# Kernel tuning notes

Hardware: AMD Instinct MI355X
Metric: run time of the kernel (lower is better)

Reference implementation:

```python
import jax, jax.numpy as jnp
import numpy as np

L, E, H, C, N = 3, 512, 8, 64, 65536
DH = E // H
LN_EPS = 1e-5


def setup_inputs() -> dict:
    key = jax.random.key(0)
    ks = jax.random.split(key, 10)
    s = 1.0 / np.sqrt(E)
    return {
        "support_features": jax.random.normal(ks[0], (N, E), jnp.float32),
        "support_labels": jax.random.randint(ks[1], (N,), 0, C),
        "W1": jax.random.normal(ks[2], (L, E, E), jnp.float32) * s,
        "b1": jnp.zeros((L, E), jnp.float32),
        "gamma": jnp.ones((L, E), jnp.float32),
        "beta": jnp.zeros((L, E), jnp.float32),
        "W2": jax.random.normal(ks[3], (L, E, E), jnp.float32) * s,
        "b2": jnp.zeros((L, E), jnp.float32),
        "Wq": jax.random.normal(ks[4], (E, E), jnp.float32) * s,
        "bq": jnp.zeros((E,), jnp.float32),
        "Wk": jax.random.normal(ks[5], (E, E), jnp.float32) * s,
        "bk": jnp.zeros((E,), jnp.float32),
        "Wv": jax.random.normal(ks[6], (E, E), jnp.float32) * s,
        "bv": jnp.zeros((E,), jnp.float32),
        "Wo": jax.random.normal(ks[7], (E, E), jnp.float32) * s,
        "bo": jnp.zeros((E,), jnp.float32),
        "level_weights": jnp.ones((L,), jnp.float32) / L,
        "level_temps": jnp.ones((L,), jnp.float32),
    }


def _layer_norm(x, g, b):
    mu = jnp.mean(x, axis=-1, keepdims=True)
    var = jnp.var(x, axis=-1, keepdims=True)
    return (x - mu) * jax.lax.rsqrt(var + LN_EPS) * g + b


def reference(support_features, support_labels, W1, b1, gamma, beta, W2, b2,
              Wq, bq, Wk, bk, Wv, bv, Wo, bo, level_weights, level_temps):
    # class membership mask [C, N]; segment counts [C]
    onehot = support_labels[None, :] == jnp.arange(C)[:, None]
    counts = jnp.sum(onehot, axis=1).astype(support_features.dtype)
    scale = 1.0 / np.sqrt(DH)
    protos = []
    for l in range(L):  # small fixed number of levels
        # prototype MLP (dropout inactive at eval)
        h = jnp.maximum(_layer_norm(support_features @ W1[l] + b1[l], gamma[l], beta[l]), 0.0)
        feat = h @ W2[l] + b2[l]                              # [N, E]
        # per-class mean context (segment mean) -> query
        ctx = (onehot.astype(feat.dtype) @ feat) / counts[:, None]  # [C, E]
        q = (ctx @ Wq + bq).reshape(C, H, DH)
        k = (feat @ Wk + bk).reshape(N, H, DH)
        v = (feat @ Wv + bv).reshape(N, H, DH)
        scores = jnp.einsum('chd,nhd->chn', q, k) * scale      # [C, H, N]
        scores = jnp.where(onehot[:, None, :], scores, -jnp.inf)
        attn = jax.nn.softmax(scores, axis=-1)
        out = jnp.einsum('chn,nhd->chd', attn, v).reshape(C, E)
        protos.append(out @ Wo + bo)                           # [C, E]
    lw = jax.nn.softmax(level_weights)
    final = protos[0] * (lw[0] / level_temps[0])
    for i in range(1, L):
        final = final + protos[i] * (lw[i] / level_temps[i])
    return final
```

## Files before the change

kernel.cpp:

```cpp
#include <hip/hip_runtime.h>
#include <math.h>

#define N_SUP 65536
#define E_DIM 512
#define H_HEADS 8
#define C_CLS 64
#define DHD 64
#define L_LEV 3
#define LN_EPS 1e-5f
#define ATTN_SPLITS 8
#define CTX_SPLITS 16
#define SCAT_BLOCKS 256
#define KV_LD 1024

typedef _Float16 f16x8 __attribute__((ext_vector_type(8)));
typedef _Float16 f16x4 __attribute__((ext_vector_type(4)));
typedef float f32x4 __attribute__((ext_vector_type(4)));

__device__ __forceinline__ void gload_lds16(const void* g, void* lds) {
    __builtin_amdgcn_global_load_lds((const __attribute__((address_space(1))) void*)g,
                                     (__attribute__((address_space(3))) void*)lds,
                                     16, 0, 0);
}

__global__ __launch_bounds__(512, 2)
void hgemm256(const _Float16* __restrict__ A, int lda, size_t aStride,
              const _Float16* __restrict__ Bt, size_t btStride,
              const float* __restrict__ bias, size_t biasStride,
              _Float16* __restrict__ C, int ldc, size_t cStride, int nCol) {
    const int z = blockIdx.y;
    A += z * aStride; Bt += z * btStride; bias += z * biasStride; C += z * cStride;

    const int nRow = gridDim.x / nCol;
    const int R = nRow < 64 ? nRow : 64;
    const int bid = blockIdx.x;
    const int bandSz = R * nCol;
    const int band = bid / bandSz;
    const int rem = bid % bandSz;
    const int colT = rem / R;
    const int rowT = band * R + (rem % R);
    const int row0 = rowT * 256, col0 = colT * 256;

    __shared__ _Float16 smem[2][2][256][64];

    const int tid = threadIdx.x;
    const int wave = tid >> 6, lane = tid & 63;
    const int wm2 = (wave & 1) * 128;
    const int wn4 = (wave >> 1) * 64;
    const int m = lane & 15, q = lane >> 4;

    const int sr = tid >> 3;
    const int sb = tid & 7;
    const int sblk = sb ^ (sr & 7);

    const _Float16* Asrc = A + (size_t)(row0 + sr) * lda + sblk * 8;
    const _Float16* Bsrc = Bt + (size_t)(col0 + sr) * E_DIM + sblk * 8;
    const size_t aPass = (size_t)64 * lda;
    const size_t bPass = (size_t)64 * E_DIM;

#define STAGE_TILE(k0, s)                                                     \
    {                                                                         \
        char* la = (char*)&smem[s][0][0][0] + wave * 1024;                    \
        char* lb = (char*)&smem[s][1][0][0] + wave * 1024;                    \
        _Pragma("unroll")                                                     \
        for (int p = 0; p < 4; ++p)                                           \
            gload_lds16(Asrc + (size_t)p * aPass + (k0), la + p * 8192);      \
        _Pragma("unroll")                                                     \
        for (int p = 0; p < 4; ++p)                                           \
            gload_lds16(Bsrc + (size_t)p * bPass + (k0), lb + p * 8192);      \
    }

    f32x4 acc[8][4];
#pragma unroll
    for (int i = 0; i < 8; ++i)
#pragma unroll
        for (int j = 0; j < 4; ++j) acc[i][j] = (f32x4){0.f, 0.f, 0.f, 0.f};

    const int c0k = ((q) ^ (m & 7)) * 8;
    const int c1k = ((4 + q) ^ (m & 7)) * 8;

    STAGE_TILE(0, 0);
    STAGE_TILE(64, 1);

    for (int t = 0; t < 8; ++t) {
        const int s = t & 1;
        if (t < 7) {
            asm volatile("s_waitcnt vmcnt(8)" ::: "memory");
        } else {
            asm volatile("s_waitcnt vmcnt(0)" ::: "memory");
        }
        __builtin_amdgcn_s_barrier();

        const _Float16* As = &smem[s][0][0][0];
        const _Float16* Bs = &smem[s][1][0][0];

        f16x8 a0[8], a1[8], b0[4], b1[4];
#pragma unroll
        for (int fr = 0; fr < 8; ++fr) {
            const int rb = (wm2 + fr * 16 + m) * 64;
            a0[fr] = *(const f16x8*)&As[rb + c0k];
            a1[fr] = *(const f16x8*)&As[rb + c1k];
        }
#pragma unroll
        for (int fc = 0; fc < 4; ++fc) {
            const int rb = (wn4 + fc * 16 + m) * 64;
            b0[fc] = *(const f16x8*)&Bs[rb + c0k];
            b1[fc] = *(const f16x8*)&Bs[rb + c1k];
        }
        asm volatile("s_waitcnt lgkmcnt(0)" ::: "memory");
        __builtin_amdgcn_s_barrier();

        if (t + 2 < 8) {
            const int k0n = (t + 2) * 64;
            STAGE_TILE(k0n, s);
        }

        __builtin_amdgcn_s_setprio(1);
#pragma unroll
        for (int fr = 0; fr < 8; ++fr)
#pragma unroll
            for (int fc = 0; fc < 4; ++fc)
                acc[fr][fc] = __builtin_amdgcn_mfma_f32_16x16x32_f16(a0[fr], b0[fc], acc[fr][fc], 0, 0, 0);
#pragma unroll
        for (int fr = 0; fr < 8; ++fr)
#pragma unroll
            for (int fc = 0; fc < 4; ++fc)
                acc[fr][fc] = __builtin_amdgcn_mfma_f32_16x16x32_f16(a1[fr], b1[fc], acc[fr][fc], 0, 0, 0);
        __builtin_amdgcn_s_setprio(0);
    }
#undef STAGE_TILE

#pragma unroll
    for (int fr = 0; fr < 8; ++fr) {
        const int rbase = row0 + wm2 + fr * 16 + q * 4;
#pragma unroll
        for (int fc = 0; fc < 4; ++fc) {
            const int col = col0 + wn4 + fc * 16 + m;
            const float bv = bias[col];
#pragma unroll
            for (int r = 0; r < 4; ++r)
                C[(size_t)(rbase + r) * ldc + col] = (_Float16)(acc[fr][fc][r] + bv);
        }
    }
}

__global__ __launch_bounds__(256)
void conv32to16(const float* __restrict__ in, _Float16* __restrict__ out, int n4) {
    int i = blockIdx.x * 256 + threadIdx.x;
    if (i < n4) {
        f32x4 v = ((const f32x4*)in)[i];
        f16x4 o = {(_Float16)v[0], (_Float16)v[1], (_Float16)v[2], (_Float16)v[3]};
        ((f16x4*)out)[i] = o;
    }
}

__global__ __launch_bounds__(256)
void transpose_all(const float* __restrict__ W1, const float* __restrict__ Wk,
                   const float* __restrict__ Wv, const float* __restrict__ Wq,
                   _Float16* __restrict__ W1allT, _Float16* __restrict__ WkvqT) {
    const int z = blockIdx.z;
    const float* src;
    _Float16* dst;
    const size_t MSZ = (size_t)E_DIM * E_DIM;
    if (z < 3)       { src = W1 + z * MSZ; dst = W1allT + z * MSZ; }
    else if (z == 3) { src = Wk;           dst = WkvqT; }
    else if (z == 4) { src = Wv;           dst = WkvqT + MSZ; }
    else             { src = Wq;           dst = WkvqT + 2 * MSZ; }

    __shared__ float t[32][33];
    const int k0 = blockIdx.x * 32, n0 = blockIdx.y * 32;
    const int tx = threadIdx.x & 31, ty = threadIdx.x >> 5;
#pragma unroll
    for (int r = 0; r < 32; r += 8)
        t[ty + r][tx] = src[(size_t)(k0 + ty + r) * E_DIM + n0 + tx];
    __syncthreads();
#pragma unroll
    for (int r = 0; r < 32; r += 8)
        dst[(size_t)(n0 + ty + r) * E_DIM + k0 + tx] = (_Float16)t[tx][ty + r];
}

__global__ __launch_bounds__(256)
void bias_compose(const float* __restrict__ b2, const float* __restrict__ Wk,
                  const float* __restrict__ Wv, const float* __restrict__ Wq,
                  const float* __restrict__ bk, const float* __restrict__ bv,
                  const float* __restrict__ bq, float* __restrict__ bcomp) {
    const int l = blockIdx.y;
    const int n = blockIdx.x * 256 + threadIdx.x;
    const float* W; const float* bb; int nn;
    if (n < 512)       { W = Wk; bb = bk; nn = n; }
    else if (n < 1024) { W = Wv; bb = bv; nn = n - 512; }
    else               { W = Wq; bb = bq; nn = n - 1024; }
    float acc = 0.f;
    for (int j = 0; j < E_DIM; ++j)
        acc = fmaf(b2[l * E_DIM + j], W[(size_t)j * E_DIM + nn], acc);
    bcomp[l * 1536 + n] = acc + bb[nn];
}

__global__ __launch_bounds__(256)
void ln_relu_all(_Float16* __restrict__ P, const float* __restrict__ gamma,
                 const float* __restrict__ beta) {
    const int row = blockIdx.x * 4 + (threadIdx.x >> 6);
    const int l = blockIdx.y;
    const int lane = threadIdx.x & 63;
    _Float16* prow = P + (size_t)row * (L_LEV * E_DIM) + l * E_DIM + lane * 8;
    const float* g = gamma + l * E_DIM + lane * 8;
    const float* b = beta  + l * E_DIM + lane * 8;
    f16x8 v = *(const f16x8*)prow;
    float x[8];
    float s = 0.f, s2 = 0.f;
#pragma unroll
    for (int e = 0; e < 8; ++e) {
        x[e] = (float)v[e];
        s += x[e];
        s2 = fmaf(x[e], x[e], s2);
    }
#pragma unroll
    for (int off = 32; off; off >>= 1) {
        s  += __shfl_xor(s, off);
        s2 += __shfl_xor(s2, off);
    }
    const float mean = s * (1.f / E_DIM);
    const float var  = s2 * (1.f / E_DIM) - mean * mean;
    const float rstd = rsqrtf(var + LN_EPS);
    f32x4 g0 = *(const f32x4*)g;
    f32x4 g1 = *(const f32x4*)(g + 4);
    f32x4 b0 = *(const f32x4*)b;
    f32x4 b1 = *(const f32x4*)(b + 4);
    f16x8 o;
#pragma unroll
    for (int e = 0; e < 4; ++e) {
        o[e]     = (_Float16)fmaxf(fmaf((x[e]     - mean) * rstd, g0[e], b0[e]), 0.f);
        o[e + 4] = (_Float16)fmaxf(fmaf((x[e + 4] - mean) * rstd, g1[e], b1[e]), 0.f);
    }
    *(f16x8*)prow = o;
}

__global__ __launch_bounds__(256)
void label_block_hist(const int* __restrict__ labels, int* __restrict__ blockCounts) {
    __shared__ int h[C_CLS];
    const int tid = threadIdx.x;
    if (tid < C_CLS) h[tid] = 0;
    __syncthreads();
    atomicAdd(&h[labels[blockIdx.x * 256 + tid]], 1);
    __syncthreads();
    if (tid < C_CLS) blockCounts[blockIdx.x * C_CLS + tid] = h[tid];
}

__global__ __launch_bounds__(64)
void scan_offsets(const int* __restrict__ blockCounts, int* __restrict__ counts,
                  int* __restrict__ offs, int* __restrict__ blockOffs) {
    const int c = threadIdx.x;
    int total = 0;
    for (int b = 0; b < SCAT_BLOCKS; ++b) total += blockCounts[b * C_CLS + c];
    counts[c] = total;
    __shared__ int tot[C_CLS];
    tot[c] = total;
    __syncthreads();
    int off = 0;
    for (int cc = 0; cc < c; ++cc) off += tot[cc];
    offs[c] = off;
    if (c == C_CLS - 1) offs[C_CLS] = off + total;
    int run = off;
    for (int b = 0; b < SCAT_BLOCKS; ++b) {
        blockOffs[b * C_CLS + c] = run;
        run += blockCounts[b * C_CLS + c];
    }
}

__global__ __launch_bounds__(256)
void scatter_sorted(const int* __restrict__ labels, const int* __restrict__ blockOffs,
                    int* __restrict__ members) {
    __shared__ int cur[C_CLS];
    const int tid = threadIdx.x;
    if (tid < C_CLS) cur[tid] = blockOffs[blockIdx.x * C_CLS + tid];
    __syncthreads();
    const int i = blockIdx.x * 256 + tid;
    const int c = labels[i];
    const int p = atomicAdd(&cur[c], 1);
    members[p] = i;
}

__global__ __launch_bounds__(256)
void zero_f32(float* __restrict__ p, int n) {
    int i = blockIdx.x * 256 + threadIdx.x;
    if (i < n) p[i] = 0.f;
}

__global__ __launch_bounds__(256)
void ctx_partial(const _Float16* __restrict__ P, const int* __restrict__ members,
                 const int* __restrict__ offsets, float* __restrict__ hpart) {
    const int c = blockIdx.x, split = blockIdx.y, l = blockIdx.z;
    const _Float16* src = P + (size_t)l * E_DIM;
    const int tid = threadIdx.x;
    const int wave = tid >> 6, lane = tid & 63;
    const int start = offsets[c], end = offsets[c + 1];
    const int wg = split * 4 + wave;
    const int stride = 4 * CTX_SPLITS;
    const int ld = L_LEV * E_DIM;

    float acc[8];
#pragma unroll
    for (int e = 0; e < 8; ++e) acc[e] = 0.f;

    int i = start + wg;
    for (; i + stride < end; i += 2 * stride) {
        const int n0 = members[i];
        const int n1 = members[i + stride];
        f16x8 r0 = *(const f16x8*)(src + (size_t)n0 * ld + lane * 8);
        f16x8 r1 = *(const f16x8*)(src + (size_t)n1 * ld + lane * 8);
#pragma unroll
        for (int e = 0; e < 8; ++e) acc[e] += (float)r0[e] + (float)r1[e];
    }
    if (i < end) {
        const int n0 = members[i];
        f16x8 r0 = *(const f16x8*)(src + (size_t)n0 * ld + lane * 8);
#pragma unroll
        for (int e = 0; e < 8; ++e) acc[e] += (float)r0[e];
    }

    __shared__ float red[4][64][8];
#pragma unroll
    for (int e = 0; e < 8; ++e) red[wave][lane][e] = acc[e];
    __syncthreads();
    float* dst = hpart + (((size_t)l * C_CLS + c) * CTX_SPLITS + split) * E_DIM;
#pragma unroll
    for (int t = 0; t < 2; ++t) {
        const int col = tid * 2 + t;
        const int ln = col >> 3, e = col & 7;
        dst[col] = red[0][ln][e] + red[1][ln][e] + red[2][ln][e] + red[3][ln][e];
    }
}

__global__ __launch_bounds__(256)
void row_gemm_q(const float* __restrict__ hpart, const int* __restrict__ counts,
                const _Float16* __restrict__ W2compT, const float* __restrict__ bcomp,
                float* __restrict__ q) {
    const int c = blockIdx.x, l = blockIdx.y;
    const int tid = threadIdx.x;
    const float inv = 1.f / (float)counts[c];
    __shared__ float xrow[E_DIM];
    const float* hp = hpart + ((size_t)l * C_CLS + c) * CTX_SPLITS * E_DIM;
    float s0 = 0.f, s1 = 0.f;
#pragma unroll
    for (int s = 0; s < CTX_SPLITS; ++s) {
        s0 += hp[s * E_DIM + tid];
        s1 += hp[s * E_DIM + tid + 256];
    }
    xrow[tid]       = s0 * inv;
    xrow[tid + 256] = s1 * inv;
    __syncthreads();

    const _Float16* Wq = W2compT + (size_t)l * 1536 * E_DIM + (size_t)1024 * E_DIM;
    const float* bias = bcomp + l * 1536 + 1024;
    const int n0 = tid, n1 = tid + 256;
    float a0 = 0.f, a1 = 0.f;
#pragma unroll 4
    for (int k0 = 0; k0 < E_DIM; k0 += 8) {
        f16x8 w0 = *(const f16x8*)(Wq + (size_t)n0 * E_DIM + k0);
        f16x8 w1 = *(const f16x8*)(Wq + (size_t)n1 * E_DIM + k0);
#pragma unroll
        for (int e = 0; e < 8; ++e) {
            const float xv = xrow[k0 + e];
            a0 = fmaf(xv, (float)w0[e], a0);
            a1 = fmaf(xv, (float)w1[e], a1);
        }
    }
    float* qq = q + (size_t)l * C_CLS * E_DIM;
    qq[c * E_DIM + n0] = a0 + bias[n0];
    qq[c * E_DIM + n1] = a1 + bias[n1];
}

__global__ __launch_bounds__(256)
void attn_partial(const float* __restrict__ q, const _Float16* __restrict__ kv,
                  const int* __restrict__ members, const int* __restrict__ offsets,
                  float* __restrict__ pm, float* __restrict__ pl,
                  float* __restrict__ po) {
    const int c = blockIdx.x, h = blockIdx.y, s = blockIdx.z;
    const int tid = threadIdx.x;
    const int wave = tid >> 6, lane = tid & 63;
    const int start = offsets[c], end = offsets[c + 1];
    const int g = s * 4 + wave;

    float qv[64];
    const bool active = (start + g * 64) < end;
    if (active) {
        const float* qrow = q + c * E_DIM + h * DHD;
#pragma unroll
        for (int d = 0; d < 64; ++d) qv[d] = qrow[d];
    }

    __shared__ float ps[4][64];
    float m = -INFINITY, lsum = 0.f, out = 0.f;

    for (int ch0 = start + g * 64; ch0 < end; ch0 += 4 * ATTN_SPLITS * 64) {
        const int nvalid = min(64, end - ch0);
        const int idx = ch0 + lane;
        const int mi = members[idx < end ? idx : end - 1];
        const _Float16* krow = kv + (size_t)mi * KV_LD + h * DHD;
        float dot = 0.f;
#pragma unroll
        for (int j = 0; j < 8; ++j) {
            f16x8 kr = *(const f16x8*)(krow + j * 8);
#pragma unroll
            for (int e = 0; e < 8; ++e)
                dot = fmaf((float)kr[e], qv[j * 8 + e], dot);
        }
        float sc = (lane < nvalid) ? dot * 0.125f : -INFINITY;
        float cm = sc;
#pragma unroll
        for (int off = 32; off; off >>= 1) cm = fmaxf(cm, __shfl_xor(cm, off));
        const float nm = fmaxf(m, cm);
        const float alpha = __expf(m - nm);
        const float p = (lane < nvalid) ? __expf(sc - nm) : 0.f;
        ps[wave][lane] = p;
        out *= alpha;
        lsum *= alpha;
        m = nm;
        asm volatile("" ::: "memory");
#pragma unroll 16
        for (int j = 0; j < 64; ++j) {
            const int nj = __shfl(mi, j);
            const float pj = ps[wave][j];
            const float vv = (float)kv[(size_t)nj * KV_LD + E_DIM + h * DHD + lane];
            out = fmaf(pj, vv, out);
            lsum += pj;
        }
    }

    __shared__ float rm[4], rl[4], racc[4][64];
    racc[wave][lane] = out;
    if (lane == 0) { rm[wave] = m; rl[wave] = lsum; }
    __syncthreads();
    if (wave == 0) {
        float M = fmaxf(fmaxf(rm[0], rm[1]), fmaxf(rm[2], rm[3]));
        float o = 0.f, Lt = 0.f;
#pragma unroll
        for (int w = 0; w < 4; ++w) {
            const float al = (rm[w] > -INFINITY) ? __expf(rm[w] - M) : 0.f;
            o  += al * racc[w][lane];
            Lt += al * rl[w];
        }
        const int pidx = (c * H_HEADS + h) * ATTN_SPLITS + s;
        po[pidx * 64 + lane] = o;
        if (lane == 0) { pm[pidx] = M; pl[pidx] = Lt; }
    }
}

__global__ __launch_bounds__(256)
void proto_accum(const float* __restrict__ pm, const float* __restrict__ pl,
                 const float* __restrict__ po, const float* __restrict__ Wo,
                 const float* __restrict__ bo, const float* __restrict__ lvlw,
                 const float* __restrict__ lvlt, int l, float* __restrict__ out) {
    const int c = blockIdx.x;
    const int tid = threadIdx.x;
    const int wave = tid >> 6, lane = tid & 63;
    __shared__ float xrow[E_DIM];
#pragma unroll
    for (int hh = wave; hh < H_HEADS; hh += 4) {
        const int ch = c * H_HEADS + hh;
        float M = -INFINITY;
#pragma unroll
        for (int s = 0; s < ATTN_SPLITS; ++s) M = fmaxf(M, pm[ch * ATTN_SPLITS + s]);
        float o = 0.f, Lt = 0.f;
#pragma unroll
        for (int s = 0; s < ATTN_SPLITS; ++s) {
            const int pidx = ch * ATTN_SPLITS + s;
            const float al = (pm[pidx] > -INFINITY) ? __expf(pm[pidx] - M) : 0.f;
            o  += al * po[pidx * 64 + lane];
            Lt += al * pl[pidx];
        }
        xrow[hh * 64 + lane] = o / Lt;
    }
    __syncthreads();

    float a0 = 0.f, a1 = 0.f;
#pragma unroll 8
    for (int k = 0; k < E_DIM; ++k) {
        float cv = xrow[k];
        a0 = fmaf(cv, Wo[(size_t)k * E_DIM + tid], a0);
        a1 = fmaf(cv, Wo[(size_t)k * E_DIM + tid + 256], a1);
    }
    float w0 = lvlw[0], w1 = lvlw[1], w2 = lvlw[2];
    float mx = fmaxf(w0, fmaxf(w1, w2));
    float e0 = expf(w0 - mx), e1 = expf(w1 - mx), e2 = expf(w2 - mx);
    float ssum = e0 + e1 + e2;
    float lw = (l == 0 ? e0 : (l == 1 ? e1 : e2)) / ssum;
    float coef = lw / lvlt[l];
    float r0 = (a0 + bo[tid]) * coef;
    float r1 = (a1 + bo[tid + 256]) * coef;
    if (l == 0) {
        out[c * E_DIM + tid]       = r0;
        out[c * E_DIM + tid + 256] = r1;
    } else {
        out[c * E_DIM + tid]       += r0;
        out[c * E_DIM + tid + 256] += r1;
    }
}

extern "C" void kernel_launch(void* const* d_in, const int* in_sizes, int n_in,
                              void* d_out, int out_size, void* d_ws, size_t ws_size,
                              hipStream_t stream) {
    const float* X      = (const float*)d_in[0];
    const int*   labels = (const int*)  d_in[1];
    const float* W1     = (const float*)d_in[2];
    const float* b1     = (const float*)d_in[3];
    const float* gamma  = (const float*)d_in[4];
    const float* beta   = (const float*)d_in[5];
    const float* W2     = (const float*)d_in[6];
    const float* b2     = (const float*)d_in[7];
    const float* Wq     = (const float*)d_in[8];
    const float* bq     = (const float*)d_in[9];
    const float* Wk     = (const float*)d_in[10];
    const float* bk     = (const float*)d_in[11];
    const float* Wv     = (const float*)d_in[12];
    const float* bv     = (const float*)d_in[13];
    const float* Wo     = (const float*)d_in[14];
    const float* bo     = (const float*)d_in[15];
    const float* lvlw   = (const float*)d_in[16];
    const float* lvlt   = (const float*)d_in[17];
    float* out = (float*)d_out;

    char* p = (char*)d_ws;
    const size_t MSZ = (size_t)E_DIM * E_DIM;
    _Float16* Xh      = (_Float16*)p; p += (size_t)N_SUP * E_DIM * 2;
    _Float16* bufPall = (_Float16*)p; p += (size_t)N_SUP * E_DIM * L_LEV * 2;
    _Float16* bufKV   = (_Float16*)p; p += (size_t)N_SUP * KV_LD * 2;
    _Float16* W1allT  = (_Float16*)p; p += L_LEV * MSZ * 2;
    _Float16* WkvqT   = (_Float16*)p; p += 3 * MSZ * 2;
    _Float16* W2f16   = (_Float16*)p; p += L_LEV * MSZ * 2;
    _Float16* W2compT = (_Float16*)p; p += (size_t)L_LEV * 1536 * E_DIM * 2;
    float* zeros512 = (float*)p; p += E_DIM * sizeof(float);
    float* bcomp = (float*)p; p += L_LEV * 1536 * sizeof(float);
    float* hpart = (float*)p; p += (size_t)L_LEV * C_CLS * CTX_SPLITS * E_DIM * sizeof(float);
    float* qb    = (float*)p; p += (size_t)L_LEV * C_CLS * E_DIM * sizeof(float);
    float* pm    = (float*)p; p += C_CLS * H_HEADS * ATTN_SPLITS * sizeof(float);
    float* pl    = (float*)p; p += C_CLS * H_HEADS * ATTN_SPLITS * sizeof(float);
    float* po    = (float*)p; p += (size_t)C_CLS * H_HEADS * ATTN_SPLITS * 64 * sizeof(float);
    int* counts      = (int*)p; p += 256;
    int* offs        = (int*)p; p += 512;
    int* members     = (int*)p; p += (size_t)N_SUP * sizeof(int);
    int* blockCounts = (int*)p; p += (size_t)SCAT_BLOCKS * C_CLS * sizeof(int);
    int* blockOffs   = (int*)p; p += (size_t)SCAT_BLOCKS * C_CLS * sizeof(int);

    label_block_hist<<<SCAT_BLOCKS, 256, 0, stream>>>(labels, blockCounts);
    scan_offsets<<<1, 64, 0, stream>>>(blockCounts, counts, offs, blockOffs);
    scatter_sorted<<<SCAT_BLOCKS, 256, 0, stream>>>(labels, blockOffs, members);

    conv32to16<<<(N_SUP * E_DIM / 4) / 256, 256, 0, stream>>>(X, Xh, N_SUP * E_DIM / 4);
    conv32to16<<<(int)(L_LEV * MSZ / 4 / 256), 256, 0, stream>>>(W2, W2f16, L_LEV * MSZ / 4);
    transpose_all<<<dim3(16, 16, 6), 256, 0, stream>>>(W1, Wk, Wv, Wq, W1allT, WkvqT);
    zero_f32<<<2, 256, 0, stream>>>(zeros512, E_DIM);

    hgemm256<<<dim3(6 * 2, L_LEV), 512, 0, stream>>>(
        WkvqT, E_DIM, 0, W2f16, MSZ, zeros512, 0,
        W2compT, E_DIM, (size_t)1536 * E_DIM, 2);
    bias_compose<<<dim3(6, L_LEV), 256, 0, stream>>>(b2, Wk, Wv, Wq, bk, bv, bq, bcomp);

    const int nRowT = N_SUP / 256;
    hgemm256<<<dim3(nRowT * 6, 1), 512, 0, stream>>>(
        Xh, E_DIM, 0, W1allT, 0, b1, 0, bufPall, L_LEV * E_DIM, 0, 6);
    ln_relu_all<<<dim3(N_SUP / 4, L_LEV), 256, 0, stream>>>(bufPall, gamma, beta);

    ctx_partial<<<dim3(C_CLS, CTX_SPLITS, L_LEV), 256, 0, stream>>>(
        bufPall, members, offs, hpart);
    row_gemm_q<<<dim3(C_CLS, L_LEV), 256, 0, stream>>>(
        hpart, counts, W2compT, bcomp, qb);

    for (int l = 0; l < L_LEV; ++l) {
        hgemm256<<<dim3(nRowT * 4, 1), 512, 0, stream>>>(
            bufPall + (size_t)l * E_DIM, L_LEV * E_DIM, 0,
            W2compT + (size_t)l * 1536 * E_DIM, 0,
            bcomp + l * 1536, 0, bufKV, KV_LD, 0, 4);
        attn_partial<<<dim3(C_CLS, H_HEADS, ATTN_SPLITS), 256, 0, stream>>>(
            qb + (size_t)l * C_CLS * E_DIM, bufKV, members, offs, pm, pl, po);
        proto_accum<<<C_CLS, 256, 0, stream>>>(pm, pl, po, Wo, bo, lvlw, lvlt, l, out);
    }
}
```

Before: 1.038 ms.

## Interleave LDS loads, global prefetch and MFMA in four sub-phases per k-tile

Restructures the fp16 MFMA GEMM main loop so each 64-wide k-tile is processed in four row-pair phases. Each phase loads a small slice of A fragments from LDS and issues part of the next tiles' global-to-LDS copies before running its MFMAs. This spreads memory traffic across the compute and reduces live A-fragment registers, at the cost of more barriers per tile and tighter vmcnt accounting.

```diff
diff --git a/kernel.cpp b/kernel.cpp
--- a/kernel.cpp
+++ b/kernel.cpp
@@ -58,17 +58,10 @@
     const size_t aPass = (size_t)64 * lda;
     const size_t bPass = (size_t)64 * E_DIM;
 
-#define STAGE_TILE(k0, s)                                                     \
-    {                                                                         \
-        char* la = (char*)&smem[s][0][0][0] + wave * 1024;                    \
-        char* lb = (char*)&smem[s][1][0][0] + wave * 1024;                    \
-        _Pragma("unroll")                                                     \
-        for (int p = 0; p < 4; ++p)                                           \
-            gload_lds16(Asrc + (size_t)p * aPass + (k0), la + p * 8192);      \
-        _Pragma("unroll")                                                     \
-        for (int p = 0; p < 4; ++p)                                           \
-            gload_lds16(Bsrc + (size_t)p * bPass + (k0), lb + p * 8192);      \
-    }
+#define SLOTA(T) ((char*)&smem[(T) & 1][0][0][0] + wave * 1024)
+#define SLOTB(T) ((char*)&smem[(T) & 1][1][0][0] + wave * 1024)
+#define STAGE_A(T, p) gload_lds16(Asrc + (size_t)(p) * aPass + (T) * 64, SLOTA(T) + (p) * 8192)
+#define STAGE_B(T, p) gload_lds16(Bsrc + (size_t)(p) * bPass + (T) * 64, SLOTB(T) + (p) * 8192)
 
     f32x4 acc[8][4];
 #pragma unroll
@@ -79,56 +72,78 @@
     const int c0k = ((q) ^ (m & 7)) * 8;
     const int c1k = ((4 + q) ^ (m & 7)) * 8;
 
-    STAGE_TILE(0, 0);
-    STAGE_TILE(64, 1);
+    STAGE_B(0, 0); STAGE_B(0, 1); STAGE_B(0, 2); STAGE_B(0, 3);
+    STAGE_A(0, 0); STAGE_A(0, 2); STAGE_A(0, 1); STAGE_A(0, 3);
+    STAGE_B(1, 0); STAGE_B(1, 1); STAGE_B(1, 2); STAGE_B(1, 3);
+    STAGE_A(1, 0); STAGE_A(1, 2);
+    asm volatile("s_waitcnt vmcnt(6)" ::: "memory");
+    __builtin_amdgcn_s_barrier();
 
     for (int t = 0; t < 8; ++t) {
-        const int s = t & 1;
-        if (t < 7) {
-            asm volatile("s_waitcnt vmcnt(8)" ::: "memory");
-        } else {
-            asm volatile("s_waitcnt vmcnt(0)" ::: "memory");
-        }
-        __builtin_amdgcn_s_barrier();
-
-        const _Float16* As = &smem[s][0][0][0];
-        const _Float16* Bs = &smem[s][1][0][0];
-
-        f16x8 a0[8], a1[8], b0[4], b1[4];
-#pragma unroll
-        for (int fr = 0; fr < 8; ++fr) {
-            const int rb = (wm2 + fr * 16 + m) * 64;
-            a0[fr] = *(const f16x8*)&As[rb + c0k];
-            a1[fr] = *(const f16x8*)&As[rb + c1k];
-        }
+        const _Float16* As = &smem[t & 1][0][0][0];
+        const _Float16* Bs = &smem[t & 1][1][0][0];
+        f16x8 b0[4], b1[4];
+        f16x8 a0[2], a1[2];
+
 #pragma unroll
         for (int fc = 0; fc < 4; ++fc) {
             const int rb = (wn4 + fc * 16 + m) * 64;
             b0[fc] = *(const f16x8*)&Bs[rb + c0k];
             b1[fc] = *(const f16x8*)&Bs[rb + c1k];
         }
+#pragma unroll
+        for (int i = 0; i < 2; ++i) {
+            const int rb = (wm2 + i * 16 + m) * 64;
+            a0[i] = *(const f16x8*)&As[rb + c0k];
+            a1[i] = *(const f16x8*)&As[rb + c1k];
+        }
+        if (t < 7) { STAGE_A(t + 1, 1); STAGE_A(t + 1, 3); }
+        __builtin_amdgcn_s_barrier();
         asm volatile("s_waitcnt lgkmcnt(0)" ::: "memory");
+        __builtin_amdgcn_s_setprio(1);
+#pragma unroll
+        for (int i = 0; i < 2; ++i)
+#pragma unroll
+            for (int fc = 0; fc < 4; ++fc) {
+                acc[i][fc] = __builtin_amdgcn_mfma_f32_16x16x32_f16(a0[i], b0[fc], acc[i][fc], 0, 0, 0);
+                acc[i][fc] = __builtin_amdgcn_mfma_f32_16x16x32_f16(a1[i], b1[fc], acc[i][fc], 0, 0, 0);
+            }
+        __builtin_amdgcn_s_setprio(0);
         __builtin_amdgcn_s_barrier();
 
-        if (t + 2 < 8) {
-            const int k0n = (t + 2) * 64;
-            STAGE_TILE(k0n, s);
-        }
-
-        __builtin_amdgcn_s_setprio(1);
-#pragma unroll
-        for (int fr = 0; fr < 8; ++fr)
-#pragma unroll
-            for (int fc = 0; fc < 4; ++fc)
-                acc[fr][fc] = __builtin_amdgcn_mfma_f32_16x16x32_f16(a0[fr], b0[fc], acc[fr][fc], 0, 0, 0);
-#pragma unroll
-        for (int fr = 0; fr < 8; ++fr)
-#pragma unroll
-            for (int fc = 0; fc < 4; ++fc)
-                acc[fr][fc] = __builtin_amdgcn_mfma_f32_16x16x32_f16(a1[fr], b1[fc], acc[fr][fc], 0, 0, 0);
-        __builtin_amdgcn_s_setprio(0);
-    }
-#undef STAGE_TILE
+#pragma unroll
+        for (int p = 1; p < 4; ++p) {
+#pragma unroll
+            for (int i = 0; i < 2; ++i) {
+                const int rb = (wm2 + (2 * p + i) * 16 + m) * 64;
+                a0[i] = *(const f16x8*)&As[rb + c0k];
+                a1[i] = *(const f16x8*)&As[rb + c1k];
+            }
+            if (p == 1) { if (t < 6) { STAGE_B(t + 2, 0); STAGE_B(t + 2, 1); } }
+            if (p == 2) { if (t < 6) { STAGE_B(t + 2, 2); STAGE_B(t + 2, 3); } }
+            if (p == 3) { if (t < 6) { STAGE_A(t + 2, 0); STAGE_A(t + 2, 2); } }
+            __builtin_amdgcn_s_barrier();
+            asm volatile("s_waitcnt lgkmcnt(0)" ::: "memory");
+            __builtin_amdgcn_s_setprio(1);
+#pragma unroll
+            for (int i = 0; i < 2; ++i)
+#pragma unroll
+                for (int fc = 0; fc < 4; ++fc) {
+                    acc[2 * p + i][fc] = __builtin_amdgcn_mfma_f32_16x16x32_f16(a0[i], b0[fc], acc[2 * p + i][fc], 0, 0, 0);
+                    acc[2 * p + i][fc] = __builtin_amdgcn_mfma_f32_16x16x32_f16(a1[i], b1[fc], acc[2 * p + i][fc], 0, 0, 0);
+                }
+            __builtin_amdgcn_s_setprio(0);
+            if (p == 3) {
+                if (t < 6)       asm volatile("s_waitcnt vmcnt(6)" ::: "memory");
+                else if (t == 6) asm volatile("s_waitcnt vmcnt(0)" ::: "memory");
+            }
+            __builtin_amdgcn_s_barrier();
+        }
+    }
+#undef STAGE_A
+#undef STAGE_B
+#undef SLOTA
+#undef SLOTB
 
 #pragma unroll
     for (int fr = 0; fr < 8; ++fr) {
```

Result: faster. 960.8 us (-7.5%).
